# Kernel optimization log

Measured on AMD Instinct MI355X. Metric: run time of the kernel, lower is better.

## Reference

```python
import jax, jax.numpy as jnp
import numpy as np

H_BEV, W_BEV, Z_LEVELS = 240, 120, 6  # BEV grid; length = Z_LEVELS*H_BEV*W_BEV = 172800


def setup_inputs() -> dict:
    key = jax.random.key(0)
    ks = jax.random.split(key, 7)
    C, H, W = 64, 256, 448
    L = Z_LEVELS * H_BEV * W_BEV  # 172800 voxels
    fish_input = jax.random.normal(ks[0], (1, 4, C, H, W), dtype=jnp.float32)
    pv_input = jax.random.normal(ks[1], (1, 1, C, H, W), dtype=jnp.float32)
    front_input = jax.random.normal(ks[2], (1, 1, C, H, W), dtype=jnp.float32)
    uu = jax.random.randint(ks[3], (6, L), 0, W)
    vv = jax.random.randint(ks[4], (6, L), 0, H)
    valid = jax.random.randint(ks[5], (6, L), 0, 2)
    density = jax.random.uniform(ks[6], (6, L), dtype=jnp.float32)
    return {"fish_input": fish_input, "pv_input": pv_input, "front_input": front_input,
            "uu": uu, "vv": vv, "valid": valid, "density": density}


def reference(fish_input, pv_input, front_input, uu, vv, valid, density):
    # Concatenate cameras: [6, C, H, W]
    feats = jnp.concatenate([fish_input[0], pv_input[0], front_input[0]], axis=0)
    n_cam, C, H, W = feats.shape
    L = uu.shape[1]
    # Gather per-voxel pixel features: flatten spatial, index by vv*W+uu
    flat = feats.reshape(n_cam, C, H * W)                 # [6, C, H*W]
    pix = (vv * W + uu).astype(jnp.int32)                 # [6, L]
    gathered = jnp.take_along_axis(flat, pix[:, None, :], axis=2)  # [6, C, L]
    # Validity mask + density weighting
    w = valid.astype(feats.dtype) * density               # [6, L]
    weighted = gathered * w[:, None, :]                   # [6, C, L]
    # Scatter-accumulate: voxels are z-major over BEV cells -> sum the Z levels per cell
    bev = weighted.reshape(n_cam, C, Z_LEVELS, H_BEV * W_BEV).sum(axis=2)
    return bev.reshape(1, n_cam * C, H_BEV, W_BEV)        # [1, 384, 240, 120]
```

## Files before the change

kernel.cpp:

```cpp
#include <hip/hip_runtime.h>

#define HW_PIX 114688
#define W_IMG  448
#define C_CH   64
#define NCAM   6
#define NCELL  28800
#define ZL     6
#define LVOX   172800

typedef unsigned int  uint32;
typedef unsigned short ushort16_t;

static __device__ __forceinline__ unsigned short f2bf(float x) {
    unsigned int u = __float_as_uint(x);
    unsigned int r = u + 0x7FFF + ((u >> 16) & 1);
    return (unsigned short)(r >> 16);
}
static __device__ __forceinline__ unsigned int pack2(float lo, float hi) {
    return (unsigned int)f2bf(lo) | ((unsigned int)f2bf(hi) << 16);
}

__global__ __launch_bounds__(256) void vp_transpose_kernel(
    const float* __restrict__ fish, const float* __restrict__ pv,
    const float* __restrict__ front, unsigned short* __restrict__ featsT)
{
    const int tilesPerCam = HW_PIX / 64;
    const int bid  = blockIdx.x;
    const int cam  = bid / tilesPerCam;
    const int pix0 = (bid % tilesPerCam) * 64;

    const float* src = (cam < 4) ? (fish + (size_t)cam * C_CH * HW_PIX)
                                 : ((cam == 4) ? pv : front);

    __shared__ float t[64][65];
    const int tid = threadIdx.x;

    #pragma unroll
    for (int i = 0; i < 4; ++i) {
        int e   = i * 256 + tid;
        int c   = e >> 4;
        int px4 = e & 15;
        const float4 f = *reinterpret_cast<const float4*>(
            src + (size_t)c * HW_PIX + pix0 + px4 * 4);
        t[c][px4 * 4 + 0] = f.x;
        t[c][px4 * 4 + 1] = f.y;
        t[c][px4 * 4 + 2] = f.z;
        t[c][px4 * 4 + 3] = f.w;
    }
    __syncthreads();

    unsigned short* dst = featsT + ((size_t)cam * HW_PIX + pix0) * C_CH;
    #pragma unroll
    for (int i = 0; i < 2; ++i) {
        int e  = i * 256 + tid;
        int px = e >> 3;
        int cg = e & 7;
        uint4 o;
        o.x = pack2(t[cg * 8 + 0][px], t[cg * 8 + 1][px]);
        o.y = pack2(t[cg * 8 + 2][px], t[cg * 8 + 3][px]);
        o.z = pack2(t[cg * 8 + 4][px], t[cg * 8 + 5][px]);
        o.w = pack2(t[cg * 8 + 6][px], t[cg * 8 + 7][px]);
        *reinterpret_cast<uint4*>(dst + (size_t)px * C_CH + cg * 8) = o;
    }
}

__global__ __launch_bounds__(256) void vp_gather_kernel(
    const unsigned short* __restrict__ featsT,
    const int*   __restrict__ uu, const int* __restrict__ vv,
    const int*   __restrict__ valid, const float* __restrict__ density,
    float* __restrict__ out)
{
    const int bid   = blockIdx.x;
    const int cam   = bid / (NCELL / 64);
    const int cell0 = (bid % (NCELL / 64)) * 64;
    const int tid   = threadIdx.x;

    __shared__ int   p_s[ZL * 64];
    __shared__ float w_s[ZL * 64];
    __shared__ float acc_s[64][65];

    for (int v = tid; v < ZL * 64; v += 256) {
        int z  = v >> 6;
        int cl = v & 63;
        size_t l = (size_t)cam * LVOX + (size_t)z * NCELL + cell0 + cl;
        p_s[v] = vv[l] * W_IMG + uu[l];
        w_s[v] = valid[l] ? density[l] : 0.0f;
    }
    __syncthreads();

    const int g    = tid >> 3;
    const int lane = tid & 7;
    const unsigned short* base =
        featsT + (size_t)cam * HW_PIX * C_CH + lane * 8;

    float acc[2][8];
    #pragma unroll
    for (int ci = 0; ci < 2; ++ci)
        #pragma unroll
        for (int k = 0; k < 8; ++k) acc[ci][k] = 0.0f;

    #pragma unroll
    for (int ci = 0; ci < 2; ++ci) {
        const int cl = g + ci * 32;
        #pragma unroll
        for (int z = 0; z < ZL; ++z) {
            const int v = z * 64 + cl;
            const float w = w_s[v];
            if (w != 0.0f) {
                const uint4 q = *reinterpret_cast<const uint4*>(
                    base + (size_t)p_s[v] * C_CH);
                acc[ci][0] += __uint_as_float(q.x << 16) * w;
                acc[ci][1] += __uint_as_float(q.x & 0xffff0000u) * w;
                acc[ci][2] += __uint_as_float(q.y << 16) * w;
                acc[ci][3] += __uint_as_float(q.y & 0xffff0000u) * w;
                acc[ci][4] += __uint_as_float(q.z << 16) * w;
                acc[ci][5] += __uint_as_float(q.z & 0xffff0000u) * w;
                acc[ci][6] += __uint_as_float(q.w << 16) * w;
                acc[ci][7] += __uint_as_float(q.w & 0xffff0000u) * w;
            }
        }
    }

    #pragma unroll
    for (int ci = 0; ci < 2; ++ci) {
        const int cl = g + ci * 32;
        #pragma unroll
        for (int k = 0; k < 8; ++k)
            acc_s[cl][lane * 8 + k] = acc[ci][k];
    }
    __syncthreads();

    #pragma unroll
    for (int i = 0; i < 4; ++i) {
        int e   = i * 256 + tid;
        int c   = e >> 4;
        int cl4 = e & 15;
        float4 f;
        f.x = acc_s[cl4 * 4 + 0][c];
        f.y = acc_s[cl4 * 4 + 1][c];
        f.z = acc_s[cl4 * 4 + 2][c];
        f.w = acc_s[cl4 * 4 + 3][c];
        *reinterpret_cast<float4*>(
            out + ((size_t)cam * C_CH + c) * NCELL + cell0 + cl4 * 4) = f;
    }
}

__global__ __launch_bounds__(256) void vp_fallback_kernel(
    const float* __restrict__ fish, const float* __restrict__ pv,
    const float* __restrict__ front,
    const int*   __restrict__ uu, const int* __restrict__ vv,
    const int*   __restrict__ valid, const float* __restrict__ density,
    float* __restrict__ out)
{
    const int idx = blockIdx.x * 256 + threadIdx.x;
    if (idx >= NCAM * C_CH * NCELL) return;
    const int cell = idx % NCELL;
    const int c    = (idx / NCELL) % C_CH;
    const int cam  = idx / (NCELL * C_CH);
    const float* src = (cam < 4)
        ? (fish + ((size_t)cam * C_CH + c) * HW_PIX)
        : (((cam == 4) ? pv : front) + (size_t)c * HW_PIX);
    float acc = 0.0f;
    for (int z = 0; z < ZL; ++z) {
        const size_t l = (size_t)cam * LVOX + (size_t)z * NCELL + cell;
        if (valid[l]) {
            acc += src[vv[l] * W_IMG + uu[l]] * density[l];
        }
    }
    out[idx] = acc;
}

extern "C" void kernel_launch(void* const* d_in, const int* in_sizes, int n_in,
                              void* d_out, int out_size, void* d_ws, size_t ws_size,
                              hipStream_t stream) {
    const float* fish    = (const float*)d_in[0];
    const float* pv      = (const float*)d_in[1];
    const float* front   = (const float*)d_in[2];
    const int*   uu      = (const int*)d_in[3];
    const int*   vv      = (const int*)d_in[4];
    const int*   valid   = (const int*)d_in[5];
    const float* density = (const float*)d_in[6];
    float*       out     = (float*)d_out;

    const size_t need = (size_t)NCAM * HW_PIX * C_CH * sizeof(unsigned short);

    if (ws_size >= need) {
        unsigned short* featsT = (unsigned short*)d_ws;
        vp_transpose_kernel<<<NCAM * (HW_PIX / 64), 256, 0, stream>>>(
            fish, pv, front, featsT);
        vp_gather_kernel<<<NCAM * (NCELL / 64), 256, 0, stream>>>(
            featsT, uu, vv, valid, density, out);
    } else {
        vp_fallback_kernel<<<(NCAM * C_CH * NCELL + 255) / 256, 256, 0, stream>>>(
            fish, pv, front, uu, vv, valid, density, out);
    }
}
```

Baseline: 74.62 us.

## Split transposed bf16 features into two 32-channel slices with wider pixel tiles

The transpose kernel now handles 256 pixels by 32 channels per block and writes two separate channel-half planes (64-byte rows) instead of one 128-byte row per pixel. Each row of the float4 source load now reads 1 KB of contiguous pixels, where it used to read 256 bytes. The gather kernel reads its per-voxel features from the two slice planes, one 16-byte quad per lane. This trades one 128-byte gather per voxel for two 64-byte gathers in different planes, which may hurt gather locality while making the transpose loads more efficient.

```diff
diff --git a/kernel.cpp b/kernel.cpp
--- a/kernel.cpp
+++ b/kernel.cpp
@@ -8,9 +8,6 @@
 #define ZL     6
 #define LVOX   172800
 
-typedef unsigned int  uint32;
-typedef unsigned short ushort16_t;
-
 static __device__ __forceinline__ unsigned short f2bf(float x) {
     unsigned int u = __float_as_uint(x);
     unsigned int r = u + 0x7FFF + ((u >> 16) & 1);
@@ -24,43 +21,47 @@
     const float* __restrict__ fish, const float* __restrict__ pv,
     const float* __restrict__ front, unsigned short* __restrict__ featsT)
 {
-    const int tilesPerCam = HW_PIX / 64;
-    const int bid  = blockIdx.x;
-    const int cam  = bid / tilesPerCam;
-    const int pix0 = (bid % tilesPerCam) * 64;
+    const int tilesPerSlice = HW_PIX / 256;
+    const int bid   = blockIdx.x;
+    const int tile  = bid % tilesPerSlice;
+    const int slice = (bid / tilesPerSlice) & 1;
+    const int cam   = bid / (tilesPerSlice * 2);
+    const int pix0  = tile * 256;
 
     const float* src = (cam < 4) ? (fish + (size_t)cam * C_CH * HW_PIX)
                                  : ((cam == 4) ? pv : front);
-
-    __shared__ float t[64][65];
+    src += (size_t)(slice * 32) * HW_PIX;
+
+    __shared__ float t[32][257];
     const int tid = threadIdx.x;
-
+    const int w   = tid >> 6;
+    const int l   = tid & 63;
+
+    #pragma unroll
+    for (int i = 0; i < 8; ++i) {
+        const int c = w + i * 4;
+        const float4 f = *reinterpret_cast<const float4*>(
+            src + (size_t)c * HW_PIX + pix0 + l * 4);
+        t[c][l * 4 + 0] = f.x;
+        t[c][l * 4 + 1] = f.y;
+        t[c][l * 4 + 2] = f.z;
+        t[c][l * 4 + 3] = f.w;
+    }
+    __syncthreads();
+
+    unsigned short* dst = featsT +
+        ((size_t)(cam * 2 + slice) * HW_PIX + pix0) * 32;
     #pragma unroll
     for (int i = 0; i < 4; ++i) {
-        int e   = i * 256 + tid;
-        int c   = e >> 4;
-        int px4 = e & 15;
-        const float4 f = *reinterpret_cast<const float4*>(
-            src + (size_t)c * HW_PIX + pix0 + px4 * 4);
-        t[c][px4 * 4 + 0] = f.x;
-        t[c][px4 * 4 + 1] = f.y;
-        t[c][px4 * 4 + 2] = f.z;
-        t[c][px4 * 4 + 3] = f.w;
-    }
-    __syncthreads();
-
-    unsigned short* dst = featsT + ((size_t)cam * HW_PIX + pix0) * C_CH;
-    #pragma unroll
-    for (int i = 0; i < 2; ++i) {
-        int e  = i * 256 + tid;
-        int px = e >> 3;
-        int cg = e & 7;
+        const int e  = i * 256 + tid;
+        const int px = e >> 2;
+        const int g  = e & 3;
         uint4 o;
-        o.x = pack2(t[cg * 8 + 0][px], t[cg * 8 + 1][px]);
-        o.y = pack2(t[cg * 8 + 2][px], t[cg * 8 + 3][px]);
-        o.z = pack2(t[cg * 8 + 4][px], t[cg * 8 + 5][px]);
-        o.w = pack2(t[cg * 8 + 6][px], t[cg * 8 + 7][px]);
-        *reinterpret_cast<uint4*>(dst + (size_t)px * C_CH + cg * 8) = o;
+        o.x = pack2(t[g * 8 + 0][px], t[g * 8 + 1][px]);
+        o.y = pack2(t[g * 8 + 2][px], t[g * 8 + 3][px]);
+        o.z = pack2(t[g * 8 + 4][px], t[g * 8 + 5][px]);
+        o.w = pack2(t[g * 8 + 6][px], t[g * 8 + 7][px]);
+        *reinterpret_cast<uint4*>(dst + (size_t)px * 32 + g * 8) = o;
     }
 }
 
@@ -88,10 +89,12 @@
     }
     __syncthreads();
 
-    const int g    = tid >> 3;
-    const int lane = tid & 7;
-    const unsigned short* base =
-        featsT + (size_t)cam * HW_PIX * C_CH + lane * 8;
+    const int g     = tid >> 3;
+    const int la    = tid & 7;
+    const int slice = la >> 2;
+    const int quad  = la & 3;
+    const unsigned short* base = featsT +
+        (size_t)(cam * 2 + slice) * HW_PIX * 32 + quad * 8;
 
     float acc[2][8];
     #pragma unroll
@@ -108,7 +111,7 @@
             const float w = w_s[v];
             if (w != 0.0f) {
                 const uint4 q = *reinterpret_cast<const uint4*>(
-                    base + (size_t)p_s[v] * C_CH);
+                    base + (size_t)p_s[v] * 32);
                 acc[ci][0] += __uint_as_float(q.x << 16) * w;
                 acc[ci][1] += __uint_as_float(q.x & 0xffff0000u) * w;
                 acc[ci][2] += __uint_as_float(q.y << 16) * w;
@@ -126,7 +129,7 @@
         const int cl = g + ci * 32;
         #pragma unroll
         for (int k = 0; k < 8; ++k)
-            acc_s[cl][lane * 8 + k] = acc[ci][k];
+            acc_s[cl][la * 8 + k] = acc[ci][k];
     }
     __syncthreads();
 
@@ -182,11 +185,11 @@
     const float* density = (const float*)d_in[6];
     float*       out     = (float*)d_out;
 
-    const size_t need = (size_t)NCAM * HW_PIX * C_CH * sizeof(unsigned short);
+    const size_t need = (size_t)NCAM * 2 * HW_PIX * 32 * sizeof(unsigned short);
 
     if (ws_size >= need) {
         unsigned short* featsT = (unsigned short*)d_ws;
-        vp_transpose_kernel<<<NCAM * (HW_PIX / 64), 256, 0, stream>>>(
+        vp_transpose_kernel<<<NCAM * 2 * (HW_PIX / 256), 256, 0, stream>>>(
             fish, pv, front, featsT);
         vp_gather_kernel<<<NCAM * (NCELL / 64), 256, 0, stream>>>(
             featsT, uu, vv, valid, density, out);
```

After: 80.27 us. 1.08x slower.
